# Kernel optimization log

Hardware: AMD Instinct MI355X
Metric: run time of the kernel (lower is better)

The kernel has to match this reference:

```python
import jax, jax.numpy as jnp
import numpy as np

B, P, K = 2, 8192, 20
ELL = 0.15          # ell_min + ell_rand
ELL_BASE = 10.0     # ell_basedist
COLOR_SCALE = 0.2
RES_MIN = 0.1       # res_mag_min
RES_MAX = 2.0       # res_mag_max
BIG = 1e10          # masking constant for invalid db points
EPS = 1e-12


def setup_inputs() -> dict:
    key = jax.random.key(0)
    ks = jax.random.split(key, 16)
    scale = jnp.array([20.0, 20.0, 60.0], jnp.float32)
    off = jnp.array([-10.0, -10.0, 1.0], jnp.float32)  # depth z in [1, 61] m
    xyz1 = jax.random.uniform(ks[0], (B, P, 3), jnp.float32) * scale + off
    xyz2 = jax.random.uniform(ks[1], (B, P, 3), jnp.float32) * scale + off
    hsv1 = jax.random.uniform(ks[2], (B, P, 3), jnp.float32)
    hsv2 = jax.random.uniform(ks[3], (B, P, 3), jnp.float32)
    n1 = jax.random.normal(ks[4], (B, P, 3), jnp.float32)
    normal1 = n1 / jnp.linalg.norm(n1, axis=-1, keepdims=True)
    n2 = jax.random.normal(ks[5], (B, P, 3), jnp.float32)
    normal2 = n2 / jnp.linalg.norm(n2, axis=-1, keepdims=True)
    nres1 = jax.random.uniform(ks[6], (B, P, 1), jnp.float32)
    nres2 = jax.random.uniform(ks[7], (B, P, 1), jnp.float32)

    def rot(k):
        a = np.asarray(jax.random.normal(k, (B, 3, 3), jnp.float32))
        q, _ = np.linalg.qr(a)
        return jnp.asarray(q, jnp.float32)

    R12 = rot(ks[8])
    R21 = rot(ks[9])
    t12 = jax.random.normal(ks[10], (B, 3, 1), jnp.float32) * 0.5
    t21 = jax.random.normal(ks[11], (B, 3, 1), jnp.float32) * 0.5
    npts1 = jax.random.randint(ks[12], (B,), P // 2, P + 1)
    npts2 = jax.random.randint(ks[13], (B,), P // 2, P + 1)
    return dict(xyz1=xyz1, xyz2=xyz2, hsv1=hsv1, hsv2=hsv2,
                normal1=normal1, normal2=normal2, nres1=nres1, nres2=nres2,
                R12=R12, t12=t12, R21=R21, t21=t21, npts1=npts1, npts2=npts2)


def _knn(pq, pdb, len_db):
    # pq [B,Pq,3], pdb [B,Pdb,3] -> squared dists [B,Pq,K], idx [B,Pq,K]
    d2 = jnp.sum((pq[:, :, None, :] - pdb[:, None, :, :]) ** 2, axis=-1)
    valid = jnp.arange(pdb.shape[1])[None, :] < len_db[:, None]
    d2 = jnp.where(valid[:, None, :], d2, BIG)
    neg, idx = jax.lax.top_k(-d2, K)
    return -neg, idx


def _gather(f, idx):
    # f [B,Pdb,C], idx [B,Pq,K] -> [B,Pq,K,C]  (knn_gather)
    return jax.vmap(lambda fb, ib: fb[ib])(f, idx)


def _transform(xyz, normal, R, t):
    x = jnp.einsum('bij,bpj->bpi', R, xyz) + t[:, :, 0][:, None, :]
    n = jnp.einsum('bij,bpj->bpi', R, normal)
    return x, n


def _side(pq, hq, nq, rq, lq, pdb, hdb, ndb, rdb, ldb):
    dists, idx = _knn(pq, pdb, ldb)                      # [B,P,K]
    # length_scale = clamp(ell*(z-base)/base, min=ell)^2
    ls = jnp.maximum(ELL * (pq[:, :, 2:3] - ELL_BASE) / ELL_BASE, ELL) ** 2
    dist_k = jnp.exp(-dists / ls)
    hsv_knn = _gather(hdb, idx)                          # [B,P,K,3]
    cdist = jnp.sqrt(jnp.sum((hq[:, :, None, :] - hsv_knn) ** 2, -1) + EPS)
    color_k = jnp.exp(-cdist / COLOR_SCALE)
    n_knn = _gather(ndb, idx)                            # [B,P,K,3]
    r_knn = _gather(rdb, idx)                            # [B,P,K,1]
    alpha = (2 * RES_MIN / (2 * RES_MIN / RES_MAX + rq[:, :, None, :] + r_knn))[..., 0]
    normal_k = jnp.maximum(jnp.sum(nq[:, :, None, :] * n_knn, -1) * alpha, 0.0)
    mask = (jnp.arange(pq.shape[1])[None, :, None] < lq[:, None, None]).astype(dist_k.dtype)
    total = jnp.sum(dist_k * color_k * normal_k * mask)
    return total / (lq.sum().astype(dist_k.dtype) * K)


def reference(xyz1, xyz2, hsv1, hsv2, normal1, normal2, nres1, nres2,
              R12, t12, R21, t21, npts1, npts2):
    x2in1, n2in1 = _transform(xyz2, normal2, R12, t12)   # pcl_gt_2_in_1
    x1in2, n1in2 = _transform(xyz1, normal1, R21, t21)   # pcl_gt_1_in_2
    k1 = _side(xyz1, hsv1, normal1, nres1, npts1, x2in1, hsv2, n2in1, nres2, npts2)
    k2 = _side(xyz2, hsv2, normal2, nres2, npts2, x1in2, hsv1, n1in2, nres1, npts1)
    return (k1 + k2) / 2
```

## Files before the change

### kernel.cpp

```cpp
#include <hip/hip_runtime.h>
#include <cstdint>
#include <cstddef>

#define PBUF 8192
#define NZB 64
#define NYB 8
#define NXB 8
#define NBINS (NZB * NYB * NXB)
#define NCOMBO 4
#define KNN 20
#define CAP 256
#define CAPB 64
#define SLOTS (NBINS * CAPB)

#define XYMIN_F (-16.0f)
#define INV_XYBINW 0.25f
#define ZMIN_F (-8.0f)
#define INV_ZBINW 0.8f

#define KEY_INF 0xFFFFFFFFFFFFFFFFull

#define THR_MULT 21.0f

#define OFF_ACCUM   0
#define OFF_DBCUR   2048
#define ZERO_BYTES  (2048 + NCOMBO * NBINS * 4)
#define OFF_DBPOS   ZERO_BYTES
#define ARR_BYTES   (NCOMBO * SLOTS * 16)
#define OFF_DBF1    (OFF_DBPOS + ARR_BYTES)
#define OFF_DBF2    (OFF_DBF1 + ARR_BYTES)

__device__ __forceinline__ int binOfZ(float z) {
  int b = (int)floorf((z - ZMIN_F) * INV_ZBINW);
  return min(max(b, 0), NZB - 1);
}
__device__ __forceinline__ int binOfXY(float v) {
  int b = (int)floorf((v - XYMIN_F) * INV_XYBINW);
  return min(max(b, 0), NXB - 1);
}

__device__ __forceinline__ float xformRow(const float* R, float tr, float x0, float x1, float x2) {
  return __fmaf_rn(R[2], x2, __fmaf_rn(R[1], x1, __fmaf_rn(R[0], x0, tr)));
}

__global__ __launch_bounds__(256) void k_scatter(
    const float* xyz1, const float* xyz2,
    const float* hsv1, const float* hsv2,
    const float* normal1, const float* normal2,
    const float* nres1, const float* nres2,
    const float* R12, const float* t12,
    const float* R21, const float* t21,
    const int* npts1, const int* npts2, char* ws) {
  int tid = blockIdx.x * 256 + threadIdx.x;
  int c = tid >> 13, j = tid & (PBUF - 1);
  int s = c >> 1, b = c & 1;
  size_t pj = (size_t)(b * PBUF + j);

  const float* dsrc = s == 0 ? xyz2 : xyz1;
  const float* dh = s == 0 ? hsv2 : hsv1;
  const float* dn = s == 0 ? normal2 : normal1;
  const float* dr = s == 0 ? nres2 : nres1;
  const float* R  = (s == 0 ? R12 : R21) + b * 9;
  const float* tt = (s == 0 ? t12 : t21) + b * 3;
  int ldb = (s == 0 ? npts2 : npts1)[b];
  if (j < ldb) {
    const float* x = dsrc + pj * 3;
    float x0 = x[0], x1 = x[1], x2 = x[2];
    float y0 = xformRow(R + 0, tt[0], x0, x1, x2);
    float y1 = xformRow(R + 3, tt[1], x0, x1, x2);
    float y2 = xformRow(R + 6, tt[2], x0, x1, x2);
    if (fabsf(y0) <= 16.0f && fabsf(y1) <= 16.0f && y2 >= -8.0f && y2 <= 72.0f) {
      const float* n = dn + pj * 3;
      float n0 = xformRow(R + 0, 0.f, n[0], n[1], n[2]);
      float n1 = xformRow(R + 3, 0.f, n[0], n[1], n[2]);
      float n2 = xformRow(R + 6, 0.f, n[0], n[1], n[2]);
      const float* h = dh + pj * 3;
      float r = dr[pj];
      int bin = (binOfZ(y2) * NYB + binOfXY(y1)) * NXB + binOfXY(y0);
      int slot = atomicAdd((int*)(ws + OFF_DBCUR) + c * NBINS + bin, 1);
      if (slot < CAPB) {
        size_t pos = (size_t)c * SLOTS + (size_t)bin * CAPB + slot;
        ((float4*)(ws + OFF_DBPOS))[pos] = make_float4(y0, y1, y2, 0.f);
        ((float4*)(ws + OFF_DBF1))[pos] = make_float4(h[0], h[1], h[2], r);
        ((float4*)(ws + OFF_DBF2))[pos] = make_float4(n0, n1, n2, 0.f);
      }
    }
  }
}

__global__ __launch_bounds__(256) void k_main(
    const float* xyz1, const float* xyz2,
    const float* hsv1, const float* hsv2,
    const float* normal1, const float* normal2,
    const float* nres1, const float* nres2,
    const int* npts1, const int* npts2, char* ws) {
  __shared__ unsigned long long sBuf[4 * (CAP + 2)];
  const int lane = threadIdx.x & 63;
  const int wIn = threadIdx.x >> 6;
  const int gw = blockIdx.x * 4 + wIn;
  const int c = gw >> 13;
  const int qi = (int)(__brev((unsigned)(gw & 8191)) >> 19);
  const int s = c >> 1, b = c & 1;
  const int lq = (s == 0 ? npts1 : npts2)[b];
  if (qi >= lq) return;

  const size_t qo = (size_t)(b * PBUF + qi);
  const float* qx = (s == 0 ? xyz1 : xyz2) + qo * 3;
  const float* qh = (s == 0 ? hsv1 : hsv2) + qo * 3;
  const float* qn = (s == 0 ? normal1 : normal2) + qo * 3;
  const float* qr = (s == 0 ? nres1 : nres2) + qo;
  const float qpx = qx[0], qpy = qx[1], qpz = qx[2];
  const float qh0 = qh[0], qh1 = qh[1], qh2 = qh[2];
  const float qn0 = qn[0], qn1 = qn[1], qn2 = qn[2];
  const float qres = qr[0];

  const float ell = fmaxf(0.015f * (qpz - 10.0f), 0.15f);
  const float ls = ell * ell;
  const float thrF = THR_MULT * ls;
  const float rad = sqrtf(thrF);
  const float inv_ls = 1.0f / ls;

  const int* C = (const int*)(ws + OFF_DBCUR) + c * NBINS;
  const int zlo = binOfZ(qpz - rad), zhi = binOfZ(qpz + rad);
  const int ylo = binOfXY(qpy - rad), yhi = binOfXY(qpy + rad);
  const int xlo = binOfXY(qpx - rad), xhi = binOfXY(qpx + rad);
  const int nxw = xhi - xlo + 1;
  const int nyx = (yhi - ylo + 1) * nxw;
  const int nseg = (zhi - zlo + 1) * nyx;

  int segS = 0, segLen = 0;
  if (lane < nseg) {
    int zi = lane / nyx, r = lane - zi * nyx;
    int yi = r / nxw, xi = r - yi * nxw;
    int bin = ((zlo + zi) * NYB + (ylo + yi)) * NXB + (xlo + xi);
    segS = bin * CAPB;
    segLen = min(C[bin], CAPB);
  }
  int cum = segLen;
  #pragma unroll
  for (int o = 1; o < 64; o <<= 1) {
    int n = __shfl_up(cum, o);
    if (lane >= o) cum += n;
  }
  const int L = __shfl(cum, 63);
  const int excl = cum - segLen;

  const float4* dbPos = (const float4*)(ws + OFF_DBPOS) + (size_t)c * SLOTS;
  const float4* dbF1  = (const float4*)(ws + OFF_DBF1) + (size_t)c * SLOTS;
  const float4* dbF2  = (const float4*)(ws + OFF_DBF2) + (size_t)c * SLOTS;

  auto computeJ = [&](int base) -> int {
    int tc = min(base + lane, L - 1);
    int kk = 0;
    #pragma unroll
    for (int step = 32; step; step >>= 1) {
      int cnd = kk + step;
      int e = __shfl(excl, cnd & 63);
      if (cnd < nseg && e <= tc) kk = cnd;
    }
    return __shfl(segS, kk) + (tc - __shfl(excl, kk));
  };

  unsigned long long* buf = sBuf + wIn * (CAP + 2);
  int pos = 0;
  if (L > 0) {
    int jc = computeJ(0);
    float4 pc = dbPos[jc];
    for (int base = 0; base < L; base += 64) {
      int j = jc;
      float4 p = pc;
      int nb = base + 64;
      if (nb < L) { jc = computeJ(nb); pc = dbPos[jc]; }
      bool in = (base + lane) < L;
      float dx = p.x - qpx, dy = p.y - qpy, dz = p.z - qpz;
      float d2 = __fmaf_rn(dx, dx, __fmaf_rn(dy, dy, dz * dz));
      bool keep = in && (d2 <= thrF);
      unsigned long long m = __ballot(keep);
      int rank = (int)__popcll(m & ((1ull << lane) - 1ull));
      if (keep) {
        int pidx = pos + rank;
        if (pidx < CAP)
          buf[pidx] = ((unsigned long long)__float_as_uint(d2) << 32) | (unsigned)j;
      }
      pos += (int)__popcll(m);
    }
    pos = min(pos, CAP);
  }

  if (lane < 2) buf[pos + lane] = KEY_INF;
  unsigned long long r0 = (lane       < pos) ? buf[lane]       : KEY_INF;
  unsigned long long r1 = (lane + 64  < pos) ? buf[lane + 64]  : KEY_INF;
  unsigned long long r2 = (lane + 128 < pos) ? buf[lane + 128] : KEY_INF;
  unsigned long long r3 = (lane + 192 < pos) ? buf[lane + 192] : KEY_INF;
  int k0 = 0, k1 = 0, k2 = 0, k3 = 0;
  const int nch = (pos + 1) >> 1;
  const ulonglong2* b2 = (const ulonglong2*)buf;
  for (int ch = 0; ch < nch; ++ch) {
    ulonglong2 q = b2[ch];
    k0 += (q.x < r0) + (q.y < r0);
    k1 += (q.x < r1) + (q.y < r1);
    k2 += (q.x < r2) + (q.y < r2);
    k3 += (q.x < r3) + (q.y < r3);
  }

  auto evalKey = [&](unsigned long long key, int rk) -> float {
    if (rk >= KNN || key == KEY_INF) return 0.f;
    int j = (int)(unsigned)key;
    float4 p = dbPos[j];
    float4 f1 = dbF1[j];
    float4 f2 = dbF2[j];
    float dx = p.x - qpx, dy = p.y - qpy, dz = p.z - qpz;
    float d2 = __fmaf_rn(dx, dx, __fmaf_rn(dy, dy, dz * dz));
    float dist_k = __expf(-d2 * inv_ls);
    float c0 = qh0 - f1.x, c1 = qh1 - f1.y, c2 = qh2 - f1.z;
    float cd = sqrtf(__fmaf_rn(c0, c0, __fmaf_rn(c1, c1, c2 * c2)) + 1e-12f);
    float color_k = __expf(cd * -5.0f);
    float alpha = 0.2f / (0.1f + qres + f1.w);
    float nd = __fmaf_rn(qn0, f2.x, __fmaf_rn(qn1, f2.y, qn2 * f2.z));
    float nk = fmaxf(nd * alpha, 0.0f);
    return dist_k * color_k * nk;
  };
  float lsum = evalKey(r0, k0) + evalKey(r1, k1) + evalKey(r2, k2) + evalKey(r3, k3);

  #pragma unroll
  for (int o = 32; o; o >>= 1) lsum += __shfl_down(lsum, o);
  if (lane == 0)
    atomicAdd((float*)(ws + OFF_ACCUM) + (s * 256 + (blockIdx.x & 255)), lsum);
}

__global__ void k_final(const int* npts1, const int* npts2, const char* ws, float* out) {
  int lane = threadIdx.x;
  const float* acc = (const float*)(ws + OFF_ACCUM);
  float s1 = acc[lane] + acc[lane + 64] + acc[lane + 128] + acc[lane + 192];
  float s2 = acc[256 + lane] + acc[256 + lane + 64] + acc[256 + lane + 128] + acc[256 + lane + 192];
  #pragma unroll
  for (int o = 32; o; o >>= 1) {
    s1 += __shfl_down(s1, o);
    s2 += __shfl_down(s2, o);
  }
  if (lane == 0) {
    float k1 = s1 / (20.0f * (float)(npts1[0] + npts1[1]));
    float k2 = s2 / (20.0f * (float)(npts2[0] + npts2[1]));
    out[0] = 0.5f * (k1 + k2);
  }
}

extern "C" void kernel_launch(void* const* d_in, const int* in_sizes, int n_in,
                              void* d_out, int out_size, void* d_ws, size_t ws_size,
                              hipStream_t stream) {
  const float* xyz1 = (const float*)d_in[0];
  const float* xyz2 = (const float*)d_in[1];
  const float* hsv1 = (const float*)d_in[2];
  const float* hsv2 = (const float*)d_in[3];
  const float* normal1 = (const float*)d_in[4];
  const float* normal2 = (const float*)d_in[5];
  const float* nres1 = (const float*)d_in[6];
  const float* nres2 = (const float*)d_in[7];
  const float* R12 = (const float*)d_in[8];
  const float* t12 = (const float*)d_in[9];
  const float* R21 = (const float*)d_in[10];
  const float* t21 = (const float*)d_in[11];
  const int* npts1 = (const int*)d_in[12];
  const int* npts2 = (const int*)d_in[13];
  char* ws = (char*)d_ws;
  float* out = (float*)d_out;

  hipMemsetAsync(ws, 0, ZERO_BYTES, stream);
  k_scatter<<<dim3(NCOMBO * PBUF / 256), dim3(256), 0, stream>>>(
      xyz1, xyz2, hsv1, hsv2, normal1, normal2, nres1, nres2,
      R12, t12, R21, t21, npts1, npts2, ws);
  k_main<<<dim3(NCOMBO * PBUF / 4), dim3(256), 0, stream>>>(
      xyz1, xyz2, hsv1, hsv2, normal1, normal2, nres1, nres2, npts1, npts2, ws);
  k_final<<<dim3(1), dim3(64), 0, stream>>>(npts1, npts2, ws, out);
}
```

Before: 117.8 us.

## Process two queries per wavefront with interleaved candidate scans

Each wavefront now handles two query points, qi and qi+4096, and interleaves their bin scans, rank counting and evaluation so that independent memory loads and shuffles overlap. The grid is halved and shared memory per block is doubled. The evaluation step also reuses the squared distance stored in the key instead of reloading the position from the database. The cost is more registers per thread and possible imbalance when the two queries have very different candidate counts.

```diff
diff --git a/kernel.cpp b/kernel.cpp
--- a/kernel.cpp
+++ b/kernel.cpp
@@ -94,133 +94,179 @@
     const float* normal1, const float* normal2,
     const float* nres1, const float* nres2,
     const int* npts1, const int* npts2, char* ws) {
-  __shared__ unsigned long long sBuf[4 * (CAP + 2)];
+  __shared__ unsigned long long sBuf[8 * (CAP + 2)];
   const int lane = threadIdx.x & 63;
   const int wIn = threadIdx.x >> 6;
   const int gw = blockIdx.x * 4 + wIn;
-  const int c = gw >> 13;
-  const int qi = (int)(__brev((unsigned)(gw & 8191)) >> 19);
+  const int c = gw >> 12;
+  const int qpair = gw & 4095;
   const int s = c >> 1, b = c & 1;
   const int lq = (s == 0 ? npts1 : npts2)[b];
-  if (qi >= lq) return;
-
-  const size_t qo = (size_t)(b * PBUF + qi);
-  const float* qx = (s == 0 ? xyz1 : xyz2) + qo * 3;
-  const float* qh = (s == 0 ? hsv1 : hsv2) + qo * 3;
-  const float* qn = (s == 0 ? normal1 : normal2) + qo * 3;
-  const float* qr = (s == 0 ? nres1 : nres2) + qo;
-  const float qpx = qx[0], qpy = qx[1], qpz = qx[2];
-  const float qh0 = qh[0], qh1 = qh[1], qh2 = qh[2];
-  const float qn0 = qn[0], qn1 = qn[1], qn2 = qn[2];
-  const float qres = qr[0];
-
-  const float ell = fmaxf(0.015f * (qpz - 10.0f), 0.15f);
-  const float ls = ell * ell;
-  const float thrF = THR_MULT * ls;
-  const float rad = sqrtf(thrF);
-  const float inv_ls = 1.0f / ls;
-
+
+  int qi[2];
+  qi[0] = (int)(__brev((unsigned)qpair) >> 20);
+  qi[1] = qi[0] + 4096;
+  const bool validB = qi[1] < lq;
+
+  const float* qxs = (s == 0 ? xyz1 : xyz2);
+  const float* qhs = (s == 0 ? hsv1 : hsv2);
+  const float* qns = (s == 0 ? normal1 : normal2);
+  const float* qrs = (s == 0 ? nres1 : nres2);
+
+  float qpx[2], qpy[2], qpz[2], qh0[2], qh1[2], qh2[2], qn0[2], qn1[2], qn2[2], qres[2];
+  float ls[2], thrF[2], inv_ls[2];
+  int nseg[2], segS[2], segLen[2], excl[2], L[2];
   const int* C = (const int*)(ws + OFF_DBCUR) + c * NBINS;
-  const int zlo = binOfZ(qpz - rad), zhi = binOfZ(qpz + rad);
-  const int ylo = binOfXY(qpy - rad), yhi = binOfXY(qpy + rad);
-  const int xlo = binOfXY(qpx - rad), xhi = binOfXY(qpx + rad);
-  const int nxw = xhi - xlo + 1;
-  const int nyx = (yhi - ylo + 1) * nxw;
-  const int nseg = (zhi - zlo + 1) * nyx;
-
-  int segS = 0, segLen = 0;
-  if (lane < nseg) {
-    int zi = lane / nyx, r = lane - zi * nyx;
-    int yi = r / nxw, xi = r - yi * nxw;
-    int bin = ((zlo + zi) * NYB + (ylo + yi)) * NXB + (xlo + xi);
-    segS = bin * CAPB;
-    segLen = min(C[bin], CAPB);
-  }
-  int cum = segLen;
-  #pragma unroll
-  for (int o = 1; o < 64; o <<= 1) {
-    int n = __shfl_up(cum, o);
-    if (lane >= o) cum += n;
-  }
-  const int L = __shfl(cum, 63);
-  const int excl = cum - segLen;
+
+  #pragma unroll
+  for (int qq = 0; qq < 2; ++qq) {
+    const size_t qo = (size_t)(b * PBUF + qi[qq]);
+    const float* qx = qxs + qo * 3;
+    const float* qh = qhs + qo * 3;
+    const float* qn = qns + qo * 3;
+    qpx[qq] = qx[0]; qpy[qq] = qx[1]; qpz[qq] = qx[2];
+    qh0[qq] = qh[0]; qh1[qq] = qh[1]; qh2[qq] = qh[2];
+    qn0[qq] = qn[0]; qn1[qq] = qn[1]; qn2[qq] = qn[2];
+    qres[qq] = qrs[qo];
+
+    const float ell = fmaxf(0.015f * (qpz[qq] - 10.0f), 0.15f);
+    ls[qq] = ell * ell;
+    thrF[qq] = THR_MULT * ls[qq];
+    const float rad = sqrtf(thrF[qq]);
+    inv_ls[qq] = 1.0f / ls[qq];
+
+    const int zlo = binOfZ(qpz[qq] - rad), zhi = binOfZ(qpz[qq] + rad);
+    const int ylo = binOfXY(qpy[qq] - rad), yhi = binOfXY(qpy[qq] + rad);
+    const int xlo = binOfXY(qpx[qq] - rad), xhi = binOfXY(qpx[qq] + rad);
+    const int nxw = xhi - xlo + 1;
+    const int nyx = (yhi - ylo + 1) * nxw;
+    nseg[qq] = (zhi - zlo + 1) * nyx;
+
+    segS[qq] = 0; segLen[qq] = 0;
+    if (lane < nseg[qq]) {
+      int zi = lane / nyx, r = lane - zi * nyx;
+      int yi = r / nxw, xi = r - yi * nxw;
+      int bin = ((zlo + zi) * NYB + (ylo + yi)) * NXB + (xlo + xi);
+      segS[qq] = bin * CAPB;
+      segLen[qq] = min(C[bin], CAPB);
+    }
+    int cum = segLen[qq];
+    #pragma unroll
+    for (int o = 1; o < 64; o <<= 1) {
+      int n = __shfl_up(cum, o);
+      if (lane >= o) cum += n;
+    }
+    L[qq] = __shfl(cum, 63);
+    excl[qq] = cum - segLen[qq];
+  }
+  if (!validB) L[1] = 0;
 
   const float4* dbPos = (const float4*)(ws + OFF_DBPOS) + (size_t)c * SLOTS;
   const float4* dbF1  = (const float4*)(ws + OFF_DBF1) + (size_t)c * SLOTS;
   const float4* dbF2  = (const float4*)(ws + OFF_DBF2) + (size_t)c * SLOTS;
 
-  auto computeJ = [&](int base) -> int {
-    int tc = min(base + lane, L - 1);
+  auto computeJ = [&](int base, int Lq, int nsegq, int exclq, int segsq) -> int {
+    int tc = min(base + lane, Lq - 1);
     int kk = 0;
     #pragma unroll
     for (int step = 32; step; step >>= 1) {
       int cnd = kk + step;
-      int e = __shfl(excl, cnd & 63);
-      if (cnd < nseg && e <= tc) kk = cnd;
-    }
-    return __shfl(segS, kk) + (tc - __shfl(excl, kk));
+      int e = __shfl(exclq, cnd & 63);
+      if (cnd < nsegq && e <= tc) kk = cnd;
+    }
+    return __shfl(segsq, kk) + (tc - __shfl(exclq, kk));
   };
 
-  unsigned long long* buf = sBuf + wIn * (CAP + 2);
-  int pos = 0;
-  if (L > 0) {
-    int jc = computeJ(0);
-    float4 pc = dbPos[jc];
-    for (int base = 0; base < L; base += 64) {
-      int j = jc;
-      float4 p = pc;
-      int nb = base + 64;
-      if (nb < L) { jc = computeJ(nb); pc = dbPos[jc]; }
-      bool in = (base + lane) < L;
-      float dx = p.x - qpx, dy = p.y - qpy, dz = p.z - qpz;
-      float d2 = __fmaf_rn(dx, dx, __fmaf_rn(dy, dy, dz * dz));
-      bool keep = in && (d2 <= thrF);
-      unsigned long long m = __ballot(keep);
-      int rank = (int)__popcll(m & ((1ull << lane) - 1ull));
-      if (keep) {
-        int pidx = pos + rank;
-        if (pidx < CAP)
-          buf[pidx] = ((unsigned long long)__float_as_uint(d2) << 32) | (unsigned)j;
+  unsigned long long* bufq[2];
+  bufq[0] = sBuf + (wIn * 2 + 0) * (CAP + 2);
+  bufq[1] = sBuf + (wIn * 2 + 1) * (CAP + 2);
+  int pos[2] = {0, 0};
+  int jc[2];
+  float4 pc[2];
+  #pragma unroll
+  for (int qq = 0; qq < 2; ++qq) {
+    if (L[qq] > 0) {
+      jc[qq] = computeJ(0, L[qq], nseg[qq], excl[qq], segS[qq]);
+      pc[qq] = dbPos[jc[qq]];
+    }
+  }
+  const int Lmax = max(L[0], L[1]);
+  for (int base = 0; base < Lmax; base += 64) {
+    #pragma unroll
+    for (int qq = 0; qq < 2; ++qq) {
+      if (base < L[qq]) {
+        int j = jc[qq];
+        float4 p = pc[qq];
+        int nb = base + 64;
+        if (nb < L[qq]) {
+          jc[qq] = computeJ(nb, L[qq], nseg[qq], excl[qq], segS[qq]);
+          pc[qq] = dbPos[jc[qq]];
+        }
+        bool in = (base + lane) < L[qq];
+        float dx = p.x - qpx[qq], dy = p.y - qpy[qq], dz = p.z - qpz[qq];
+        float d2 = __fmaf_rn(dx, dx, __fmaf_rn(dy, dy, dz * dz));
+        bool keep = in && (d2 <= thrF[qq]);
+        unsigned long long m = __ballot(keep);
+        int rank = (int)__popcll(m & ((1ull << lane) - 1ull));
+        if (keep) {
+          int pidx = pos[qq] + rank;
+          if (pidx < CAP)
+            bufq[qq][pidx] = ((unsigned long long)__float_as_uint(d2) << 32) | (unsigned)j;
+        }
+        pos[qq] += (int)__popcll(m);
       }
-      pos += (int)__popcll(m);
-    }
-    pos = min(pos, CAP);
-  }
-
-  if (lane < 2) buf[pos + lane] = KEY_INF;
-  unsigned long long r0 = (lane       < pos) ? buf[lane]       : KEY_INF;
-  unsigned long long r1 = (lane + 64  < pos) ? buf[lane + 64]  : KEY_INF;
-  unsigned long long r2 = (lane + 128 < pos) ? buf[lane + 128] : KEY_INF;
-  unsigned long long r3 = (lane + 192 < pos) ? buf[lane + 192] : KEY_INF;
-  int k0 = 0, k1 = 0, k2 = 0, k3 = 0;
-  const int nch = (pos + 1) >> 1;
-  const ulonglong2* b2 = (const ulonglong2*)buf;
-  for (int ch = 0; ch < nch; ++ch) {
-    ulonglong2 q = b2[ch];
-    k0 += (q.x < r0) + (q.y < r0);
-    k1 += (q.x < r1) + (q.y < r1);
-    k2 += (q.x < r2) + (q.y < r2);
-    k3 += (q.x < r3) + (q.y < r3);
-  }
-
-  auto evalKey = [&](unsigned long long key, int rk) -> float {
-    if (rk >= KNN || key == KEY_INF) return 0.f;
-    int j = (int)(unsigned)key;
-    float4 p = dbPos[j];
-    float4 f1 = dbF1[j];
-    float4 f2 = dbF2[j];
-    float dx = p.x - qpx, dy = p.y - qpy, dz = p.z - qpz;
-    float d2 = __fmaf_rn(dx, dx, __fmaf_rn(dy, dy, dz * dz));
-    float dist_k = __expf(-d2 * inv_ls);
-    float c0 = qh0 - f1.x, c1 = qh1 - f1.y, c2 = qh2 - f1.z;
-    float cd = sqrtf(__fmaf_rn(c0, c0, __fmaf_rn(c1, c1, c2 * c2)) + 1e-12f);
-    float color_k = __expf(cd * -5.0f);
-    float alpha = 0.2f / (0.1f + qres + f1.w);
-    float nd = __fmaf_rn(qn0, f2.x, __fmaf_rn(qn1, f2.y, qn2 * f2.z));
-    float nk = fmaxf(nd * alpha, 0.0f);
-    return dist_k * color_k * nk;
-  };
-  float lsum = evalKey(r0, k0) + evalKey(r1, k1) + evalKey(r2, k2) + evalKey(r3, k3);
+    }
+  }
+  pos[0] = min(pos[0], CAP);
+  pos[1] = min(pos[1], CAP);
+
+  unsigned long long r0[2], r1[2], r2[2], r3[2];
+  int k0[2] = {0, 0}, k1[2] = {0, 0}, k2[2] = {0, 0}, k3[2] = {0, 0};
+  int nch[2];
+  #pragma unroll
+  for (int qq = 0; qq < 2; ++qq) {
+    if (lane < 2) bufq[qq][pos[qq] + lane] = KEY_INF;
+    r0[qq] = (lane       < pos[qq]) ? bufq[qq][lane]       : KEY_INF;
+    r1[qq] = (lane + 64  < pos[qq]) ? bufq[qq][lane + 64]  : KEY_INF;
+    r2[qq] = (lane + 128 < pos[qq]) ? bufq[qq][lane + 128] : KEY_INF;
+    r3[qq] = (lane + 192 < pos[qq]) ? bufq[qq][lane + 192] : KEY_INF;
+    nch[qq] = (pos[qq] + 1) >> 1;
+  }
+  const int nchmax = max(nch[0], nch[1]);
+  for (int ch = 0; ch < nchmax; ++ch) {
+    #pragma unroll
+    for (int qq = 0; qq < 2; ++qq) {
+      if (ch < nch[qq]) {
+        ulonglong2 q = ((const ulonglong2*)bufq[qq])[ch];
+        k0[qq] += (q.x < r0[qq]) + (q.y < r0[qq]);
+        k1[qq] += (q.x < r1[qq]) + (q.y < r1[qq]);
+        k2[qq] += (q.x < r2[qq]) + (q.y < r2[qq]);
+        k3[qq] += (q.x < r3[qq]) + (q.y < r3[qq]);
+      }
+    }
+  }
+
+  float lsum = 0.f;
+  #pragma unroll
+  for (int qq = 0; qq < 2; ++qq) {
+    auto evalKey = [&](unsigned long long key, int rk) -> float {
+      if (rk >= KNN || key == KEY_INF) return 0.f;
+      int j = (int)(unsigned)key;
+      float d2 = __uint_as_float((unsigned)(key >> 32));
+      float4 f1 = dbF1[j];
+      float4 f2 = dbF2[j];
+      float dist_k = __expf(-d2 * inv_ls[qq]);
+      float c0 = qh0[qq] - f1.x, c1 = qh1[qq] - f1.y, c2 = qh2[qq] - f1.z;
+      float cd = sqrtf(__fmaf_rn(c0, c0, __fmaf_rn(c1, c1, c2 * c2)) + 1e-12f);
+      float color_k = __expf(cd * -5.0f);
+      float alpha = 0.2f / (0.1f + qres[qq] + f1.w);
+      float nd = __fmaf_rn(qn0[qq], f2.x, __fmaf_rn(qn1[qq], f2.y, qn2[qq] * f2.z));
+      float nk = fmaxf(nd * alpha, 0.0f);
+      return dist_k * color_k * nk;
+    };
+    lsum += evalKey(r0[qq], k0[qq]) + evalKey(r1[qq], k1[qq])
+          + evalKey(r2[qq], k2[qq]) + evalKey(r3[qq], k3[qq]);
+  }
 
   #pragma unroll
   for (int o = 32; o; o >>= 1) lsum += __shfl_down(lsum, o);
@@ -269,7 +315,7 @@
   k_scatter<<<dim3(NCOMBO * PBUF / 256), dim3(256), 0, stream>>>(
       xyz1, xyz2, hsv1, hsv2, normal1, normal2, nres1, nres2,
       R12, t12, R21, t21, npts1, npts2, ws);
-  k_main<<<dim3(NCOMBO * PBUF / 4), dim3(256), 0, stream>>>(
+  k_main<<<dim3(NCOMBO * PBUF / 8), dim3(256), 0, stream>>>(
       xyz1, xyz2, hsv1, hsv2, normal1, normal2, nres1, nres2, npts1, npts2, ws);
   k_final<<<dim3(1), dim3(64), 0, stream>>>(npts1, npts2, ws, out);
 }
```

Result: faster. 111.8 us (-5.1%).
